# Kernel optimization log

Hardware: AMD Instinct MI355X
Metric: run time of the kernel (lower is better)

The kernel has to match this reference:

```python
import jax, jax.numpy as jnp
import numpy as np

N_NODES = 50000
N_EDGES = 800000
N_GRAPHS = 512
HIDDEN = 256
NODE_FEAT = 9
LAYERS = 4


def setup_inputs() -> dict:
    key = jax.random.key(0)
    ks = jax.random.split(key, 9)
    x = jax.random.normal(ks[0], (N_NODES, NODE_FEAT), dtype=jnp.float32)
    edge_index = jax.random.randint(ks[1], (2, N_EDGES), 0, N_NODES, dtype=jnp.int64)
    batch = jnp.sort(jax.random.randint(ks[2], (N_NODES,), 0, N_GRAPHS, dtype=jnp.int64))
    embed_W = jax.random.normal(ks[3], (NODE_FEAT, HIDDEN), dtype=jnp.float32) * (1.0 / np.sqrt(NODE_FEAT))
    embed_b = jnp.zeros((HIDDEN,), dtype=jnp.float32)
    conv_W = jax.random.normal(ks[4], (LAYERS, HIDDEN, HIDDEN), dtype=jnp.float32) * (1.0 / np.sqrt(HIDDEN))
    conv_b = jnp.zeros((LAYERS, HIDDEN), dtype=jnp.float32)
    out_W = jax.random.normal(ks[5], (HIDDEN, 1), dtype=jnp.float32) * (1.0 / np.sqrt(HIDDEN))
    out_b = jnp.zeros((1,), dtype=jnp.float32)
    return {"x": x, "edge_index": edge_index, "batch": batch,
            "embed_W": embed_W, "embed_b": embed_b,
            "conv_W": conv_W, "conv_b": conv_b,
            "out_W": out_W, "out_b": out_b}


def reference(x, edge_index, batch, embed_W, embed_b, conv_W, conv_b, out_W, out_b):
    n = x.shape[0]
    src, dst = edge_index[0], edge_index[1]
    # GCN symmetric normalization with self-loops: deg includes the self-loop (+1)
    deg = jax.ops.segment_sum(jnp.ones(src.shape[0], x.dtype), dst, num_segments=n) + 1.0
    dinv = jax.lax.rsqrt(deg)                       # [N]
    norm_e = dinv[src] * dinv[dst]                  # [E] edge coefficient
    self_coef = (dinv * dinv)[:, None]              # [N,1] self-loop coefficient

    h = jax.nn.relu(x @ embed_W + embed_b)          # [N,H]
    for l in range(conv_W.shape[0]):
        hw = h @ conv_W[l]                          # [N,H] transform first
        msg = hw[src] * norm_e[:, None]             # [E,H] gather + scale
        agg = jax.ops.segment_sum(msg, dst, num_segments=n)  # scatter-add
        agg = agg + hw * self_coef                  # self-loop contribution
        h = jax.nn.relu(agg + conv_b[l])

    # global mean pool over graph ids
    sums = jax.ops.segment_sum(h, batch, num_segments=N_GRAPHS)           # [G,H]
    cnt = jax.ops.segment_sum(jnp.ones(n, h.dtype), batch, num_segments=N_GRAPHS)
    pooled = sums / jnp.maximum(cnt, 1.0)[:, None]
    return pooled @ out_W + out_b                   # [G,1]
```

## Files before the change

kernel.cpp:

```cpp
#include <hip/hip_runtime.h>

#define N_NODES 50000
#define N_EDGES 800000
#define N_GRAPHS 512
#define HIDDEN 256
#define NODE_FEAT 9
#define LAYERS 4
#define BUCKET 64
#define NSLICE 8

typedef float floatx4 __attribute__((ext_vector_type(4)));
typedef short short8 __attribute__((ext_vector_type(8)));

__device__ __forceinline__ float bf2f(unsigned u) {
    unsigned v = u << 16;
    float f;
    __builtin_memcpy(&f, &v, 4);
    return f;
}
__device__ __forceinline__ unsigned short f2bf(float f) {
    unsigned v;
    __builtin_memcpy(&v, &f, 4);
    v += 0x7FFFu + ((v >> 16) & 1u);
    return (unsigned short)(v >> 16);
}
__device__ __forceinline__ size_t smb(int s, int n) {
    return ((size_t)s * N_NODES + (size_t)n) * 32;
}

__global__ void fillb_kernel(const int* __restrict__ src, const int* __restrict__ dst,
                             int* __restrict__ cnt, int* __restrict__ col_src, int E) {
    int e = blockIdx.x * blockDim.x + threadIdx.x;
    if (e < E) {
        int d = dst[e];
        int pos = atomicAdd(&cnt[d], 1);
        if (pos < BUCKET) col_src[d * BUCKET + pos] = src[e];
    }
}

__global__ __launch_bounds__(256) void aux_kernel(const int* __restrict__ cnt,
                                                  float* __restrict__ dinv,
                                                  const int* __restrict__ batch,
                                                  int* __restrict__ gstart) {
    int i = blockIdx.x * 256 + threadIdx.x;
    if (i < N_NODES) dinv[i] = rsqrtf((float)(cnt[i] + 1));
    int g = i - N_NODES;
    if (g >= 0 && g <= N_GRAPHS) {
        if (g == N_GRAPHS) { gstart[g] = N_NODES; return; }
        int lo = 0, hi = N_NODES;
        while (lo < hi) {
            int mid = (lo + hi) >> 1;
            if (batch[mid] < g) lo = mid + 1; else hi = mid;
        }
        gstart[g] = lo;
    }
}

__global__ __launch_bounds__(256) void packW_kernel(const float* __restrict__ W,
                                                    unsigned short* __restrict__ Wsw) {
    int idx = blockIdx.x * 256 + threadIdx.x;
    int lane = idx & 63;
    int ct   = (idx >> 6) & 15;
    int ks   = (idx >> 10) & 7;
    int l    = idx >> 13;
    int n = ct * 16 + (lane & 15);
    int kbase = ks * 32 + (lane >> 4) * 8;
    const float* Wl = W + (size_t)l * HIDDEN * HIDDEN;
    alignas(16) unsigned short tmp[8];
    #pragma unroll
    for (int j = 0; j < 8; j++)
        tmp[j] = f2bf(Wl[(size_t)(kbase + j) * HIDDEN + n]);
    *(uint4*)&Wsw[(size_t)idx * 8] = *(const uint4*)tmp;
}

__global__ __launch_bounds__(256, 3) void embed_gemm(const float* __restrict__ x,
                                                     const float* __restrict__ embW,
                                                     const float* __restrict__ embb,
                                                     const unsigned short* __restrict__ Wsw,
                                                     unsigned short* __restrict__ hwout, int N) {
    __shared__ unsigned short As[64][264];
    int t = threadIdx.x;
    int wv = t >> 6, lane = t & 63, quad = lane >> 4, l15 = lane & 15;
    int n0 = blockIdx.x * 64;

    const short8* Wl = (const short8*)Wsw;
    short8 bq[2][4];
    #pragma unroll
    for (int ci = 0; ci < 4; ci++)
        bq[0][ci] = Wl[(size_t)(wv * 4 + ci) * 64 + lane];

    #pragma unroll 2
    for (int i = 0; i < 8; i++) {
        int j = t + i * 256;
        int r = j >> 5;
        int c8 = j & 31;
        int n = n0 + r;
        unsigned o0 = 0, o1 = 0, o2 = 0, o3 = 0;
        if (n < N) {
            float xr[NODE_FEAT];
            #pragma unroll
            for (int k = 0; k < NODE_FEAT; k++) xr[k] = x[(size_t)n * NODE_FEAT + k];
            float4 a0 = *(const float4*)&embb[c8 * 8];
            float4 a1 = *(const float4*)&embb[c8 * 8 + 4];
            #pragma unroll
            for (int k = 0; k < NODE_FEAT; k++) {
                float4 w0 = *(const float4*)&embW[k * HIDDEN + c8 * 8];
                float4 w1 = *(const float4*)&embW[k * HIDDEN + c8 * 8 + 4];
                a0.x += xr[k] * w0.x; a0.y += xr[k] * w0.y;
                a0.z += xr[k] * w0.z; a0.w += xr[k] * w0.w;
                a1.x += xr[k] * w1.x; a1.y += xr[k] * w1.y;
                a1.z += xr[k] * w1.z; a1.w += xr[k] * w1.w;
            }
            o0 = (unsigned)f2bf(fmaxf(a0.x, 0.f)) | ((unsigned)f2bf(fmaxf(a0.y, 0.f)) << 16);
            o1 = (unsigned)f2bf(fmaxf(a0.z, 0.f)) | ((unsigned)f2bf(fmaxf(a0.w, 0.f)) << 16);
            o2 = (unsigned)f2bf(fmaxf(a1.x, 0.f)) | ((unsigned)f2bf(fmaxf(a1.y, 0.f)) << 16);
            o3 = (unsigned)f2bf(fmaxf(a1.z, 0.f)) | ((unsigned)f2bf(fmaxf(a1.w, 0.f)) << 16);
        }
        *(uint4*)&As[r][c8 * 8] = make_uint4(o0, o1, o2, o3);
    }
    __syncthreads();

    floatx4 acc[4][4];
    #pragma unroll
    for (int i = 0; i < 4; i++)
        #pragma unroll
        for (int j = 0; j < 4; j++)
            acc[i][j] = (floatx4){0.f, 0.f, 0.f, 0.f};

    #pragma unroll
    for (int ks = 0; ks < 8; ks++) {
        if (ks < 7) {
            #pragma unroll
            for (int ci = 0; ci < 4; ci++)
                bq[(ks + 1) & 1][ci] = Wl[(size_t)((ks + 1) * 16 + wv * 4 + ci) * 64 + lane];
        }
        short8 a[4];
        #pragma unroll
        for (int rt = 0; rt < 4; rt++)
            a[rt] = *(const short8*)&As[rt * 16 + l15][ks * 32 + quad * 8];
        #pragma unroll
        for (int rt = 0; rt < 4; rt++)
            #pragma unroll
            for (int ci = 0; ci < 4; ci++)
                acc[rt][ci] = __builtin_amdgcn_mfma_f32_16x16x32_bf16(a[rt], bq[ks & 1][ci], acc[rt][ci], 0, 0, 0);
    }

    __syncthreads();
    #pragma unroll
    for (int rt = 0; rt < 4; rt++) {
        #pragma unroll
        for (int ci = 0; ci < 4; ci++) {
            int col = (wv * 4 + ci) * 16 + l15;
            int rowb = rt * 16 + quad * 4;
            #pragma unroll
            for (int reg = 0; reg < 4; reg++)
                As[rowb + reg][col] = f2bf(acc[rt][ci][reg]);
        }
    }
    __syncthreads();
    #pragma unroll
    for (int i = 0; i < 8; i++) {
        int j = t + i * 256;
        int r = j >> 5;
        int c = j & 31;
        int n = n0 + r;
        if (n < N)
            *(uint4*)&hwout[smb(c >> 2, n) + (c & 3) * 8] = *(const uint4*)&As[r][c * 8];
    }
}

__global__ __launch_bounds__(256, 3) void gemm_mfma(const unsigned short* __restrict__ hin,
                                                    const unsigned short* __restrict__ Wsw,
                                                    unsigned short* __restrict__ hwout, int N) {
    __shared__ unsigned short As[64][264];
    int t = threadIdx.x;
    int wv = t >> 6, lane = t & 63, quad = lane >> 4, l15 = lane & 15;
    int n0 = blockIdx.x * 64;

    uint4 av[8];
    #pragma unroll
    for (int i = 0; i < 8; i++) {
        int j = t + i * 256;
        int r = j >> 5;
        int c = j & 31;
        int n = n0 + r;
        av[i] = make_uint4(0u, 0u, 0u, 0u);
        if (n < N) av[i] = *(const uint4*)&hin[smb(c >> 2, n) + (c & 3) * 8];
    }
    const short8* Wl = (const short8*)Wsw;
    short8 bq[2][4];
    #pragma unroll
    for (int ci = 0; ci < 4; ci++)
        bq[0][ci] = Wl[(size_t)(wv * 4 + ci) * 64 + lane];
    #pragma unroll
    for (int i = 0; i < 8; i++) {
        int j = t + i * 256;
        int r = j >> 5;
        int c = j & 31;
        *(uint4*)&As[r][c * 8] = av[i];
    }
    __syncthreads();

    floatx4 acc[4][4];
    #pragma unroll
    for (int i = 0; i < 4; i++)
        #pragma unroll
        for (int j = 0; j < 4; j++)
            acc[i][j] = (floatx4){0.f, 0.f, 0.f, 0.f};

    #pragma unroll
    for (int ks = 0; ks < 8; ks++) {
        if (ks < 7) {
            #pragma unroll
            for (int ci = 0; ci < 4; ci++)
                bq[(ks + 1) & 1][ci] = Wl[(size_t)((ks + 1) * 16 + wv * 4 + ci) * 64 + lane];
        }
        short8 a[4];
        #pragma unroll
        for (int rt = 0; rt < 4; rt++)
            a[rt] = *(const short8*)&As[rt * 16 + l15][ks * 32 + quad * 8];
        #pragma unroll
        for (int rt = 0; rt < 4; rt++)
            #pragma unroll
            for (int ci = 0; ci < 4; ci++)
                acc[rt][ci] = __builtin_amdgcn_mfma_f32_16x16x32_bf16(a[rt], bq[ks & 1][ci], acc[rt][ci], 0, 0, 0);
    }

    __syncthreads();
    #pragma unroll
    for (int rt = 0; rt < 4; rt++) {
        #pragma unroll
        for (int ci = 0; ci < 4; ci++) {
            int col = (wv * 4 + ci) * 16 + l15;
            int rowb = rt * 16 + quad * 4;
            #pragma unroll
            for (int reg = 0; reg < 4; reg++)
                As[rowb + reg][col] = f2bf(acc[rt][ci][reg]);
        }
    }
    __syncthreads();
    #pragma unroll
    for (int i = 0; i < 8; i++) {
        int j = t + i * 256;
        int r = j >> 5;
        int c = j & 31;
        int n = n0 + r;
        if (n < N)
            *(uint4*)&hwout[smb(c >> 2, n) + (c & 3) * 8] = *(const uint4*)&As[r][c * 8];
    }
}

__global__ __launch_bounds__(256) void agg_kernel(const unsigned short* __restrict__ hw,
                                                  const int* __restrict__ cnt,
                                                  const int* __restrict__ col_src,
                                                  const float* __restrict__ dinv,
                                                  const float* __restrict__ bias,
                                                  unsigned short* __restrict__ hout) {
    __shared__ uint2 sEdge[4][4][BUCKET];
    int t = threadIdx.x;
    int wv = t >> 6, lane = t & 63;
    int sub = lane >> 4, cl = lane & 15;
    int slice = blockIdx.x & 7;
    int chunk = blockIdx.x >> 3;
    int n = chunk * 16 + wv * 4 + sub;
    float dn = dinv[n];
    int deg = cnt[n]; if (deg > BUCKET) deg = BUCKET;

    #pragma unroll
    for (int r = 0; r < 4; r++) {
        int e = cl + r * 16;
        if (e < deg) {
            int s = col_src[n * BUCKET + e];
            float nr = dinv[s] * dn;
            unsigned nrb; __builtin_memcpy(&nrb, &nr, 4);
            sEdge[wv][sub][e] = make_uint2((unsigned)s, nrb);
        }
    }

    size_t sb = smb(slice, n);
    unsigned su = *(const unsigned*)&hw[sb + 2 * cl];
    float2 b2 = *(const float2*)&bias[slice * 32 + 2 * cl];
    float selfc = dn * dn;
    float a0 = bf2f(su & 0xFFFFu) * selfc + b2.x;
    float a1 = bf2f(su >> 16)     * selfc + b2.y;

    size_t slice_base = (size_t)slice * N_NODES;
    for (int i = 0; i < deg; i++) {
        uint2 p = sEdge[wv][sub][i];
        float nr; __builtin_memcpy(&nr, &p.y, 4);
        unsigned u = *(const unsigned*)&hw[(slice_base + p.x) * 32 + 2 * cl];
        a0 += nr * bf2f(u & 0xFFFFu);
        a1 += nr * bf2f(u >> 16);
    }
    unsigned o = (unsigned)f2bf(fmaxf(a0, 0.0f)) | ((unsigned)f2bf(fmaxf(a1, 0.0f)) << 16);
    *(unsigned*)&hout[sb + 2 * cl] = o;
}

__global__ __launch_bounds__(256) void agg_dot_kernel(const unsigned short* __restrict__ hw,
                                                      const int* __restrict__ cnt,
                                                      const int* __restrict__ col_src,
                                                      const float* __restrict__ dinv,
                                                      const float* __restrict__ bias,
                                                      const float* __restrict__ outW,
                                                      float* __restrict__ dotp) {
    __shared__ uint2 sEdge[4][4][BUCKET];
    int t = threadIdx.x;
    int wv = t >> 6, lane = t & 63;
    int sub = lane >> 4, cl = lane & 15;
    int slice = blockIdx.x & 7;
    int chunk = blockIdx.x >> 3;
    int n = chunk * 16 + wv * 4 + sub;
    float dn = dinv[n];
    int deg = cnt[n]; if (deg > BUCKET) deg = BUCKET;

    #pragma unroll
    for (int r = 0; r < 4; r++) {
        int e = cl + r * 16;
        if (e < deg) {
            int s = col_src[n * BUCKET + e];
            float nr = dinv[s] * dn;
            unsigned nrb; __builtin_memcpy(&nrb, &nr, 4);
            sEdge[wv][sub][e] = make_uint2((unsigned)s, nrb);
        }
    }

    size_t sb = smb(slice, n);
    unsigned su = *(const unsigned*)&hw[sb + 2 * cl];
    float2 b2 = *(const float2*)&bias[slice * 32 + 2 * cl];
    float selfc = dn * dn;
    float a0 = bf2f(su & 0xFFFFu) * selfc + b2.x;
    float a1 = bf2f(su >> 16)     * selfc + b2.y;

    size_t slice_base = (size_t)slice * N_NODES;
    for (int i = 0; i < deg; i++) {
        uint2 p = sEdge[wv][sub][i];
        float nr; __builtin_memcpy(&nr, &p.y, 4);
        unsigned u = *(const unsigned*)&hw[(slice_base + p.x) * 32 + 2 * cl];
        a0 += nr * bf2f(u & 0xFFFFu);
        a1 += nr * bf2f(u >> 16);
    }
    float2 w2 = *(const float2*)&outW[slice * 32 + 2 * cl];
    float dot = fmaxf(a0, 0.0f) * w2.x + fmaxf(a1, 0.0f) * w2.y;
    #pragma unroll
    for (int off = 8; off > 0; off >>= 1) dot += __shfl_xor(dot, off, 64);
    if (cl == 0) dotp[(size_t)n * NSLICE + slice] = dot;
}

__global__ __launch_bounds__(64) void finalize_kernel(const float* __restrict__ dotp,
                                                      const int* __restrict__ gstart,
                                                      const float* __restrict__ outb,
                                                      float* __restrict__ out) {
    int g = blockIdx.x;
    int lane = threadIdx.x;
    int s = gstart[g], e = gstart[g + 1];
    float acc = 0.0f;
    for (size_t i = (size_t)s * NSLICE + lane; i < (size_t)e * NSLICE; i += 64) acc += dotp[i];
    #pragma unroll
    for (int off = 32; off > 0; off >>= 1) acc += __shfl_xor(acc, off, 64);
    if (lane == 0) out[g] = acc / fmaxf((float)(e - s), 1.0f) + outb[0];
}

extern "C" void kernel_launch(void* const* d_in, const int* in_sizes, int n_in,
                              void* d_out, int out_size, void* d_ws, size_t ws_size,
                              hipStream_t stream) {
    const float* x     = (const float*)d_in[0];
    const int*   edge  = (const int*)d_in[1];
    const int*   src   = edge;
    const int*   dst   = edge + N_EDGES;
    const int*   batch = (const int*)d_in[2];
    const float* embW  = (const float*)d_in[3];
    const float* embb  = (const float*)d_in[4];
    const float* convW = (const float*)d_in[5];
    const float* convb = (const float*)d_in[6];
    const float* outW  = (const float*)d_in[7];
    const float* outb  = (const float*)d_in[8];
    float* out = (float*)d_out;

    char* ws = (char*)d_ws;
    size_t off = 0;
    auto take = [&](size_t bytes) { char* p = ws + off; off += (bytes + 255) & ~(size_t)255; return p; };
    int*   cnt     = (int*)  take((size_t)N_NODES * 4);
    int*   col_src = (int*)  take((size_t)N_NODES * BUCKET * 4);
    float* dinv    = (float*)take((size_t)N_NODES * 4);
    int*   gstart  = (int*)  take((size_t)(N_GRAPHS + 1) * 4);
    float* dotp    = (float*)take((size_t)N_NODES * NSLICE * 4);
    unsigned short* Wsw = (unsigned short*)take((size_t)LAYERS * 8 * 16 * 64 * 8 * 2);
    unsigned short* h0  = (unsigned short*)take((size_t)N_NODES * HIDDEN * 2);
    unsigned short* h1  = (unsigned short*)take((size_t)N_NODES * HIDDEN * 2);

    hipMemsetAsync(cnt, 0, (size_t)N_NODES * 4, stream);

    packW_kernel<<<128, 256, 0, stream>>>(convW, Wsw);
    fillb_kernel<<<(N_EDGES + 255) / 256, 256, 0, stream>>>(src, dst, cnt, col_src, N_EDGES);
    aux_kernel<<<(N_NODES + N_GRAPHS + 1 + 255) / 256, 256, 0, stream>>>(cnt, dinv, batch, gstart);

    int nblk = (N_NODES + 63) / 64;
    int ablk = (N_NODES / 16) * NSLICE;

    embed_gemm<<<nblk, 256, 0, stream>>>(x, embW, embb, Wsw, h1, N_NODES);
    agg_kernel<<<ablk, 256, 0, stream>>>(h1, cnt, col_src, dinv, convb + 0 * HIDDEN, h0);
    gemm_mfma<<<nblk, 256, 0, stream>>>(h0, Wsw + (size_t)1 * 65536, h1, N_NODES);
    agg_kernel<<<ablk, 256, 0, stream>>>(h1, cnt, col_src, dinv, convb + 1 * HIDDEN, h0);
    gemm_mfma<<<nblk, 256, 0, stream>>>(h0, Wsw + (size_t)2 * 65536, h1, N_NODES);
    agg_kernel<<<ablk, 256, 0, stream>>>(h1, cnt, col_src, dinv, convb + 2 * HIDDEN, h0);
    gemm_mfma<<<nblk, 256, 0, stream>>>(h0, Wsw + (size_t)3 * 65536, h1, N_NODES);
    agg_dot_kernel<<<ablk, 256, 0, stream>>>(h1, cnt, col_src, dinv, convb + 3 * HIDDEN, outW, dotp);

    finalize_kernel<<<N_GRAPHS, 64, 0, stream>>>(dotp, gstart, outb, out);
}
```

Before: 518.3 us.

## Precompute edge (src, norm) pairs once and unroll gather loop in aggregation

Result: faster. 476.6 us (-8.0%).

```diff
diff --git a/kernel.cpp b/kernel.cpp
--- a/kernel.cpp
+++ b/kernel.cpp
@@ -56,6 +56,21 @@
     }
 }
 
+__global__ __launch_bounds__(256) void eprep_kernel(const int* __restrict__ cnt,
+                                                    const int* __restrict__ col_src,
+                                                    const float* __restrict__ dinv,
+                                                    uint2* __restrict__ esrc) {
+    int i = blockIdx.x * 256 + threadIdx.x;
+    int n = i >> 6, e = i & 63;
+    int deg = cnt[n]; if (deg > BUCKET) deg = BUCKET;
+    if (e < deg) {
+        int s = col_src[i];
+        float nr = dinv[s] * dinv[n];
+        unsigned nrb; __builtin_memcpy(&nrb, &nr, 4);
+        esrc[i] = make_uint2((unsigned)s, nrb);
+    }
+}
+
 __global__ __launch_bounds__(256) void packW_kernel(const float* __restrict__ W,
                                                     unsigned short* __restrict__ Wsw) {
     int idx = blockIdx.x * 256 + threadIdx.x;
@@ -160,12 +175,11 @@
     __syncthreads();
     #pragma unroll
     for (int i = 0; i < 8; i++) {
-        int j = t + i * 256;
-        int r = j >> 5;
-        int c = j & 31;
+        int r = t >> 2;
+        int oct = t & 3;
         int n = n0 + r;
         if (n < N)
-            *(uint4*)&hwout[smb(c >> 2, n) + (c & 3) * 8] = *(const uint4*)&As[r][c * 8];
+            *(uint4*)&hwout[smb(i, n) + oct * 8] = *(const uint4*)&As[r][i * 32 + oct * 8];
     }
 }
 
@@ -176,16 +190,15 @@
     int t = threadIdx.x;
     int wv = t >> 6, lane = t & 63, quad = lane >> 4, l15 = lane & 15;
     int n0 = blockIdx.x * 64;
+    int sr = t >> 2;
+    int soct = t & 3;
 
     uint4 av[8];
     #pragma unroll
     for (int i = 0; i < 8; i++) {
-        int j = t + i * 256;
-        int r = j >> 5;
-        int c = j & 31;
-        int n = n0 + r;
+        int n = n0 + sr;
         av[i] = make_uint4(0u, 0u, 0u, 0u);
-        if (n < N) av[i] = *(const uint4*)&hin[smb(c >> 2, n) + (c & 3) * 8];
+        if (n < N) av[i] = *(const uint4*)&hin[smb(i, n) + soct * 8];
     }
     const short8* Wl = (const short8*)Wsw;
     short8 bq[2][4];
@@ -193,12 +206,8 @@
     for (int ci = 0; ci < 4; ci++)
         bq[0][ci] = Wl[(size_t)(wv * 4 + ci) * 64 + lane];
     #pragma unroll
-    for (int i = 0; i < 8; i++) {
-        int j = t + i * 256;
-        int r = j >> 5;
-        int c = j & 31;
-        *(uint4*)&As[r][c * 8] = av[i];
-    }
+    for (int i = 0; i < 8; i++)
+        *(uint4*)&As[sr][i * 32 + soct * 8] = av[i];
     __syncthreads();
 
     floatx4 acc[4][4];
@@ -241,18 +250,15 @@
     __syncthreads();
     #pragma unroll
     for (int i = 0; i < 8; i++) {
-        int j = t + i * 256;
-        int r = j >> 5;
-        int c = j & 31;
-        int n = n0 + r;
+        int n = n0 + sr;
         if (n < N)
-            *(uint4*)&hwout[smb(c >> 2, n) + (c & 3) * 8] = *(const uint4*)&As[r][c * 8];
+            *(uint4*)&hwout[smb(i, n) + soct * 8] = *(const uint4*)&As[sr][i * 32 + soct * 8];
     }
 }
 
 __global__ __launch_bounds__(256) void agg_kernel(const unsigned short* __restrict__ hw,
                                                   const int* __restrict__ cnt,
-                                                  const int* __restrict__ col_src,
+                                                  const uint2* __restrict__ esrc,
                                                   const float* __restrict__ dinv,
                                                   const float* __restrict__ bias,
                                                   unsigned short* __restrict__ hout) {
@@ -269,36 +275,52 @@
     #pragma unroll
     for (int r = 0; r < 4; r++) {
         int e = cl + r * 16;
-        if (e < deg) {
-            int s = col_src[n * BUCKET + e];
-            float nr = dinv[s] * dn;
-            unsigned nrb; __builtin_memcpy(&nrb, &nr, 4);
-            sEdge[wv][sub][e] = make_uint2((unsigned)s, nrb);
-        }
-    }
-
-    size_t sb = smb(slice, n);
-    unsigned su = *(const unsigned*)&hw[sb + 2 * cl];
+        if (e < deg) sEdge[wv][sub][e] = esrc[n * BUCKET + e];
+    }
+
+    const unsigned short* hws = hw + smb(slice, 0);
+    const unsigned short* hwl = hws + 2 * cl;
+
+    unsigned su = *(const unsigned*)(hws + (size_t)n * 32 + 2 * cl);
     float2 b2 = *(const float2*)&bias[slice * 32 + 2 * cl];
     float selfc = dn * dn;
     float a0 = bf2f(su & 0xFFFFu) * selfc + b2.x;
     float a1 = bf2f(su >> 16)     * selfc + b2.y;
 
-    size_t slice_base = (size_t)slice * N_NODES;
-    for (int i = 0; i < deg; i++) {
+    int i = 0;
+    for (; i + 4 <= deg; i += 4) {
+        uint2 p0 = sEdge[wv][sub][i];
+        uint2 p1 = sEdge[wv][sub][i + 1];
+        uint2 p2 = sEdge[wv][sub][i + 2];
+        uint2 p3 = sEdge[wv][sub][i + 3];
+        unsigned u0 = *(const unsigned*)(hwl + (size_t)p0.x * 32);
+        unsigned u1 = *(const unsigned*)(hwl + (size_t)p1.x * 32);
+        unsigned u2 = *(const unsigned*)(hwl + (size_t)p2.x * 32);
+        unsigned u3 = *(const unsigned*)(hwl + (size_t)p3.x * 32);
+        float n0_, n1_, n2_, n3_;
+        __builtin_memcpy(&n0_, &p0.y, 4);
+        __builtin_memcpy(&n1_, &p1.y, 4);
+        __builtin_memcpy(&n2_, &p2.y, 4);
+        __builtin_memcpy(&n3_, &p3.y, 4);
+        a0 += n0_ * bf2f(u0 & 0xFFFFu); a1 += n0_ * bf2f(u0 >> 16);
+        a0 += n1_ * bf2f(u1 & 0xFFFFu); a1 += n1_ * bf2f(u1 >> 16);
+        a0 += n2_ * bf2f(u2 & 0xFFFFu); a1 += n2_ * bf2f(u2 >> 16);
+        a0 += n3_ * bf2f(u3 & 0xFFFFu); a1 += n3_ * bf2f(u3 >> 16);
+    }
+    for (; i < deg; i++) {
         uint2 p = sEdge[wv][sub][i];
         float nr; __builtin_memcpy(&nr, &p.y, 4);
-        unsigned u = *(const unsigned*)&hw[(slice_base + p.x) * 32 + 2 * cl];
+        unsigned u = *(const unsigned*)(hwl + (size_t)p.x * 32);
         a0 += nr * bf2f(u & 0xFFFFu);
         a1 += nr * bf2f(u >> 16);
     }
     unsigned o = (unsigned)f2bf(fmaxf(a0, 0.0f)) | ((unsigned)f2bf(fmaxf(a1, 0.0f)) << 16);
-    *(unsigned*)&hout[sb + 2 * cl] = o;
+    *(unsigned*)&hout[smb(slice, n) + 2 * cl] = o;
 }
 
 __global__ __launch_bounds__(256) void agg_dot_kernel(const unsigned short* __restrict__ hw,
                                                       const int* __restrict__ cnt,
-                                                      const int* __restrict__ col_src,
+                                                      const uint2* __restrict__ esrc,
                                                       const float* __restrict__ dinv,
                                                       const float* __restrict__ bias,
                                                       const float* __restrict__ outW,
@@ -316,26 +338,42 @@
     #pragma unroll
     for (int r = 0; r < 4; r++) {
         int e = cl + r * 16;
-        if (e < deg) {
-            int s = col_src[n * BUCKET + e];
-            float nr = dinv[s] * dn;
-            unsigned nrb; __builtin_memcpy(&nrb, &nr, 4);
-            sEdge[wv][sub][e] = make_uint2((unsigned)s, nrb);
-        }
-    }
-
-    size_t sb = smb(slice, n);
-    unsigned su = *(const unsigned*)&hw[sb + 2 * cl];
+        if (e < deg) sEdge[wv][sub][e] = esrc[n * BUCKET + e];
+    }
+
+    const unsigned short* hws = hw + smb(slice, 0);
+    const unsigned short* hwl = hws + 2 * cl;
+
+    unsigned su = *(const unsigned*)(hws + (size_t)n * 32 + 2 * cl);
     float2 b2 = *(const float2*)&bias[slice * 32 + 2 * cl];
     float selfc = dn * dn;
     float a0 = bf2f(su & 0xFFFFu) * selfc + b2.x;
     float a1 = bf2f(su >> 16)     * selfc + b2.y;
 
-    size_t slice_base = (size_t)slice * N_NODES;
-    for (int i = 0; i < deg; i++) {
+    int i = 0;
+    for (; i + 4 <= deg; i += 4) {
+        uint2 p0 = sEdge[wv][sub][i];
+        uint2 p1 = sEdge[wv][sub][i + 1];
+        uint2 p2 = sEdge[wv][sub][i + 2];
+        uint2 p3 = sEdge[wv][sub][i + 3];
+        unsigned u0 = *(const unsigned*)(hwl + (size_t)p0.x * 32);
+        unsigned u1 = *(const unsigned*)(hwl + (size_t)p1.x * 32);
+        unsigned u2 = *(const unsigned*)(hwl + (size_t)p2.x * 32);
+        unsigned u3 = *(const unsigned*)(hwl + (size_t)p3.x * 32);
+        float n0_, n1_, n2_, n3_;
+        __builtin_memcpy(&n0_, &p0.y, 4);
+        __builtin_memcpy(&n1_, &p1.y, 4);
+        __builtin_memcpy(&n2_, &p2.y, 4);
+        __builtin_memcpy(&n3_, &p3.y, 4);
+        a0 += n0_ * bf2f(u0 & 0xFFFFu); a1 += n0_ * bf2f(u0 >> 16);
+        a0 += n1_ * bf2f(u1 & 0xFFFFu); a1 += n1_ * bf2f(u1 >> 16);
+        a0 += n2_ * bf2f(u2 & 0xFFFFu); a1 += n2_ * bf2f(u2 >> 16);
+        a0 += n3_ * bf2f(u3 & 0xFFFFu); a1 += n3_ * bf2f(u3 >> 16);
+    }
+    for (; i < deg; i++) {
         uint2 p = sEdge[wv][sub][i];
         float nr; __builtin_memcpy(&nr, &p.y, 4);
-        unsigned u = *(const unsigned*)&hw[(slice_base + p.x) * 32 + 2 * cl];
+        unsigned u = *(const unsigned*)(hwl + (size_t)p.x * 32);
         a0 += nr * bf2f(u & 0xFFFFu);
         a1 += nr * bf2f(u >> 16);
     }
@@ -381,6 +419,7 @@
     auto take = [&](size_t bytes) { char* p = ws + off; off += (bytes + 255) & ~(size_t)255; return p; };
     int*   cnt     = (int*)  take((size_t)N_NODES * 4);
     int*   col_src = (int*)  take((size_t)N_NODES * BUCKET * 4);
+    uint2* esrc    = (uint2*)take((size_t)N_NODES * BUCKET * 8);
     float* dinv    = (float*)take((size_t)N_NODES * 4);
     int*   gstart  = (int*)  take((size_t)(N_GRAPHS + 1) * 4);
     float* dotp    = (float*)take((size_t)N_NODES * NSLICE * 4);
@@ -393,18 +432,19 @@
     packW_kernel<<<128, 256, 0, stream>>>(convW, Wsw);
     fillb_kernel<<<(N_EDGES + 255) / 256, 256, 0, stream>>>(src, dst, cnt, col_src, N_EDGES);
     aux_kernel<<<(N_NODES + N_GRAPHS + 1 + 255) / 256, 256, 0, stream>>>(cnt, dinv, batch, gstart);
+    eprep_kernel<<<(N_NODES * BUCKET) / 256, 256, 0, stream>>>(cnt, col_src, dinv, esrc);
 
     int nblk = (N_NODES + 63) / 64;
     int ablk = (N_NODES / 16) * NSLICE;
 
     embed_gemm<<<nblk, 256, 0, stream>>>(x, embW, embb, Wsw, h1, N_NODES);
-    agg_kernel<<<ablk, 256, 0, stream>>>(h1, cnt, col_src, dinv, convb + 0 * HIDDEN, h0);
+    agg_kernel<<<ablk, 256, 0, stream>>>(h1, cnt, esrc, dinv, convb + 0 * HIDDEN, h0);
     gemm_mfma<<<nblk, 256, 0, stream>>>(h0, Wsw + (size_t)1 * 65536, h1, N_NODES);
-    agg_kernel<<<ablk, 256, 0, stream>>>(h1, cnt, col_src, dinv, convb + 1 * HIDDEN, h0);
+    agg_kernel<<<ablk, 256, 0, stream>>>(h1, cnt, esrc, dinv, convb + 1 * HIDDEN, h0);
     gemm_mfma<<<nblk, 256, 0, stream>>>(h0, Wsw + (size_t)2 * 65536, h1, N_NODES);
-    agg_kernel<<<ablk, 256, 0, stream>>>(h1, cnt, col_src, dinv, convb + 2 * HIDDEN, h0);
+    agg_kernel<<<ablk, 256, 0, stream>>>(h1, cnt, esrc, dinv, convb + 2 * HIDDEN, h0);
     gemm_mfma<<<nblk, 256, 0, stream>>>(h0, Wsw + (size_t)3 * 65536, h1, N_NODES);
-    agg_dot_kernel<<<ablk, 256, 0, stream>>>(h1, cnt, col_src, dinv, convb + 3 * HIDDEN, outW, dotp);
+    agg_dot_kernel<<<ablk, 256, 0, stream>>>(h1, cnt, esrc, dinv, convb + 3 * HIDDEN, outW, dotp);
 
     finalize_kernel<<<N_GRAPHS, 64, 0, stream>>>(dotp, gstart, outb, out);
 }
```
